# Performance work log

Measured on AMD Instinct MI355X. Metric: run time of the kernel, lower is better.

## Reference

```python
import jax, jax.numpy as jnp
import numpy as np

N = 100000   # nodes
E = 800000   # edges
D = 128      # input dim
H = 128      # hidden dim
C = 2        # output classes
BN_EPS = 1e-5


def setup_inputs() -> dict:
    key = jax.random.key(0)
    ks = jax.random.split(key, 24)
    glorot = lambda k, shape: jax.random.normal(k, shape, dtype=jnp.float32) * np.sqrt(2.0 / (shape[0] + shape[1]))
    inp = {
        "x": jax.random.normal(ks[0], (N, D), dtype=jnp.float32),
        "edge_index": jax.random.randint(ks[1], (2, E), 0, N, dtype=jnp.int64),
        "W0": glorot(ks[2], (D, H)), "b0": jnp.zeros((H,), jnp.float32),
        "W1": glorot(ks[3], (H, H)), "b1": jnp.zeros((H,), jnp.float32),
        "W2": glorot(ks[4], (H, H)), "b2": jnp.zeros((H,), jnp.float32),
        "W3": glorot(ks[5], (H, C)), "b3": jnp.zeros((C,), jnp.float32),
        # BatchNorm (eval mode: running stats)
        "bn0_g": jax.random.normal(ks[6], (H,), dtype=jnp.float32) * 0.1 + 1.0,
        "bn0_b": jax.random.normal(ks[7], (H,), dtype=jnp.float32) * 0.1,
        "bn0_m": jax.random.normal(ks[8], (H,), dtype=jnp.float32) * 0.1,
        "bn0_v": jax.random.uniform(ks[9], (H,), dtype=jnp.float32) + 0.5,
        "bn1_g": jax.random.normal(ks[10], (H,), dtype=jnp.float32) * 0.1 + 1.0,
        "bn1_b": jax.random.normal(ks[11], (H,), dtype=jnp.float32) * 0.1,
        "bn1_m": jax.random.normal(ks[12], (H,), dtype=jnp.float32) * 0.1,
        "bn1_v": jax.random.uniform(ks[13], (H,), dtype=jnp.float32) + 0.5,
    }
    return inp


def _gcn_conv(h, W, b, src, dst, norm, self_norm):
    # GCNConv: D^-1/2 (A + I) D^-1/2 (h W) + b
    hw = h @ W                                             # [N, out]
    msg = hw[src] * norm[:, None]                          # [E, out] gather
    agg = jax.ops.segment_sum(msg, dst, num_segments=N)    # [N, out] scatter-add
    return agg + hw * self_norm[:, None] + b


def _bn_eval(h, g, b, m, v):
    return (h - m) * (g * jax.lax.rsqrt(v + BN_EPS)) + b


def reference(x, edge_index, W0, b0, W1, b1, W2, b2, W3, b3,
              bn0_g, bn0_b, bn0_m, bn0_v, bn1_g, bn1_b, bn1_m, bn1_v):
    src, dst = edge_index[0], edge_index[1]
    # symmetric normalization with self-loops
    deg = jax.ops.segment_sum(jnp.ones((E,), jnp.float32), dst, num_segments=N) + 1.0
    dis = jax.lax.rsqrt(deg)                 # deg >= 1, no inf
    norm = dis[src] * dis[dst]               # per-edge norm
    self_norm = dis * dis                    # self-loop norm

    # layer 0 (eval mode: dropout is identity)
    h = jax.nn.relu(_gcn_conv(x, W0, b0, src, dst, norm, self_norm))
    # layer 1: conv -> bn -> relu -> residual
    h_prev = h
    h = _gcn_conv(h, W1, b1, src, dst, norm, self_norm)
    h = jax.nn.relu(_bn_eval(h, bn0_g, bn0_b, bn0_m, bn0_v)) + h_prev
    # layer 2
    h_prev = h
    h = _gcn_conv(h, W2, b2, src, dst, norm, self_norm)
    h = jax.nn.relu(_bn_eval(h, bn1_g, bn1_b, bn1_m, bn1_v)) + h_prev
    # output layer
    h = _gcn_conv(h, W3, b3, src, dst, norm, self_norm)
    return jax.nn.log_softmax(h, axis=1)
```

## Files before the change

kernel.cpp:

```cpp
#include <hip/hip_runtime.h>
#include <hip/hip_bf16.h>
#include <type_traits>

#define NN 100000
#define NE 800000
#define HD 128
#define BN_EPS 1e-5f
#define NB_E_C 3125

typedef __bf16 bf16x8 __attribute__((ext_vector_type(8)));
typedef __bf16 bf16x2 __attribute__((ext_vector_type(2)));
typedef float  f32x4  __attribute__((ext_vector_type(4)));
typedef float  f32x2  __attribute__((ext_vector_type(2)));


__global__ __launch_bounds__(256) void count_prep_k(const int* __restrict__ ei, int* __restrict__ count,
                                                    int* __restrict__ rank,
                                                    const float* __restrict__ W0, const float* __restrict__ W1,
                                                    const float* __restrict__ W2, __bf16* __restrict__ WT,
                                                    const float* __restrict__ g0, const float* __restrict__ b0,
                                                    const float* __restrict__ m0, const float* __restrict__ v0,
                                                    const float* __restrict__ g1, const float* __restrict__ b1,
                                                    const float* __restrict__ m1, const float* __restrict__ v1,
                                                    float* __restrict__ A0, float* __restrict__ B0,
                                                    float* __restrict__ A1, float* __restrict__ B1) {
    int bid = blockIdx.x;
    int tid = threadIdx.x;
    if (bid < NB_E_C) {
        int e = bid * 256 + tid;
        if (e < NE) rank[e] = atomicAdd(&count[ei[NE + e]], 1);
    } else if (bid < NB_E_C + 3) {
        int w = bid - NB_E_C;
        const float* Ws[3] = {W0, W1, W2};
        const float* W = Ws[w];
        __bf16* T = WT + w * (HD * HD);
        #pragma unroll 4
        for (int it = 0; it < 64; ++it) {
            int idx = it * 256 + tid;
            int n = idx >> 7, k = idx & 127;
            T[idx] = (__bf16)W[k * HD + n];
        }
    } else {
        if (tid < 128) {
            float a = g0[tid] * rsqrtf(v0[tid] + BN_EPS);
            A0[tid] = a; B0[tid] = b0[tid] - m0[tid] * a;
        } else {
            int u = tid - 128;
            float a = g1[u] * rsqrtf(v1[u] + BN_EPS);
            A1[u] = a; B1[u] = b1[u] - m1[u] * a;
        }
    }
}

__global__ __launch_bounds__(256) void scan1_k(const int* __restrict__ count,
                                               int* __restrict__ rp, int* __restrict__ bsums,
                                               float* __restrict__ dis, float* __restrict__ selfn) {
    __shared__ int sm[256];
    int tid = threadIdx.x;
    int i = blockIdx.x * 256 + tid;
    int v = (i < NN) ? count[i] : 0;
    if (i < NN) {
        float deg = (float)v + 1.0f;
        float di = rsqrtf(deg);
        dis[i] = di;
        selfn[i] = di * di;
    }
    sm[tid] = v; __syncthreads();
    for (int off = 1; off < 256; off <<= 1) {
        int t = (tid >= off) ? sm[tid - off] : 0;
        __syncthreads();
        sm[tid] += t;
        __syncthreads();
    }
    if (i < NN) rp[i] = sm[tid] - v;
    if (tid == 255) bsums[blockIdx.x] = sm[tid];
}

__global__ __launch_bounds__(256) void scan23_k(int* __restrict__ rp, const int* __restrict__ bsums, int nb) {
    __shared__ int sm[256];
    int tid = threadIdx.x;
    int b = blockIdx.x;
    int partial = 0;
    for (int i = tid; i < b; i += 256) partial += bsums[i];
    sm[tid] = partial; __syncthreads();
    #pragma unroll
    for (int off = 128; off > 0; off >>= 1) {
        if (tid < off) sm[tid] += sm[tid + off];
        __syncthreads();
    }
    int prefix = sm[0];
    int i = b * 256 + tid;
    if (i < NN) rp[i] += prefix;
    if (i == 0) rp[NN] = NE;
}

__global__ __launch_bounds__(256) void scatter_k(const int* __restrict__ ei, const int* __restrict__ rp,
                                                 const int* __restrict__ rank, const float* __restrict__ dis,
                                                 uint2* __restrict__ edges) {
    int e = blockIdx.x * 256 + threadIdx.x;
    if (e >= NE) return;
    int s = ei[e], d = ei[NE + e];
    int pos = rp[d] + rank[e];
    edges[pos] = make_uint2((unsigned)s, __float_as_uint(dis[s] * dis[d]));
}


template <typename T>
__global__ __launch_bounds__(256, 5) void gemm128_k(const T* __restrict__ A, const __bf16* __restrict__ WTg,
                                                    __bf16* __restrict__ HW) {
    __shared__ __bf16 WL[128 * 128];
    const int tid = threadIdx.x;
    const int wid  = __builtin_amdgcn_readfirstlane(tid >> 6);
    const int lane = tid & 63;
    const int m = lane & 15, quad = lane >> 4;
    const int row_base = blockIdx.x * 64 + wid * 16;

    int r = row_base + m;
    if (r >= NN) r = NN - 1;
    bf16x8 afr[4];
    if constexpr (std::is_same<T, float>::value) {
        const float4* ap = (const float4*)(A + (size_t)r * HD);
        #pragma unroll
        for (int ks = 0; ks < 4; ++ks) {
            float4 x0 = ap[ks * 8 + quad * 2], x1 = ap[ks * 8 + quad * 2 + 1];
            bf16x8 a;
            a[0] = (__bf16)x0.x; a[1] = (__bf16)x0.y; a[2] = (__bf16)x0.z; a[3] = (__bf16)x0.w;
            a[4] = (__bf16)x1.x; a[5] = (__bf16)x1.y; a[6] = (__bf16)x1.z; a[7] = (__bf16)x1.w;
            afr[ks] = a;
        }
    } else {
        const bf16x8* ap = (const bf16x8*)(A + (size_t)r * HD);
        #pragma unroll
        for (int ks = 0; ks < 4; ++ks) afr[ks] = ap[ks * 4 + quad];
    }

    #pragma unroll
    for (int it = 0; it < 8; ++it) {
        int id = it * 256 + tid;
        int n = id >> 4, c = id & 15;
        int cs = c ^ (n >> 3);
        *(uint4*)&WL[n * 128 + cs * 8] = *(const uint4*)(WTg + n * HD + c * 8);
    }
    __syncthreads();

    f32x4 acc[8];
    #pragma unroll
    for (int ct = 0; ct < 8; ++ct) acc[ct] = (f32x4){0.f, 0.f, 0.f, 0.f};

    #pragma unroll
    for (int ks = 0; ks < 4; ++ks) {
        #pragma unroll
        for (int ct = 0; ct < 8; ++ct) {
            int n = m * 8 + ct;
            int cs = (ks * 4 + quad) ^ m;
            bf16x8 bfr = *(const bf16x8*)&WL[n * 128 + cs * 8];
            acc[ct] = __builtin_amdgcn_mfma_f32_16x16x32_bf16(afr[ks], bfr, acc[ct], 0, 0, 0);
        }
    }

    #pragma unroll
    for (int rr = 0; rr < 4; ++rr) {
        int row = row_base + quad * 4 + rr;
        if (row < NN) {
            bf16x8 v;
            #pragma unroll
            for (int ct = 0; ct < 8; ++ct) v[ct] = (__bf16)acc[ct][rr];
            *(bf16x8*)(HW + (size_t)row * HD + m * 8) = v;
        }
    }
}


__device__ __forceinline__ void acc8p(f32x2* acc, uint4 rv, float wt) {
    f32x2 w2 = {wt, wt};
    f32x2 x0 = {__uint_as_float(rv.x << 16), __uint_as_float(rv.x & 0xffff0000u)};
    f32x2 x1 = {__uint_as_float(rv.y << 16), __uint_as_float(rv.y & 0xffff0000u)};
    f32x2 x2 = {__uint_as_float(rv.z << 16), __uint_as_float(rv.z & 0xffff0000u)};
    f32x2 x3 = {__uint_as_float(rv.w << 16), __uint_as_float(rv.w & 0xffff0000u)};
    acc[0] = __builtin_elementwise_fma(x0, w2, acc[0]);
    acc[1] = __builtin_elementwise_fma(x1, w2, acc[1]);
    acc[2] = __builtin_elementwise_fma(x2, w2, acc[2]);
    acc[3] = __builtin_elementwise_fma(x3, w2, acc[3]);
}


__global__ __launch_bounds__(256) void agg0_k(const __bf16* __restrict__ hw, const int* __restrict__ rp,
                                              const uint2* __restrict__ edges,
                                              const float* __restrict__ selfn, const float* __restrict__ bias,
                                              __bf16* __restrict__ hb) {
    const int lane = threadIdx.x & 63;
    const int wid  = threadIdx.x >> 6;
    const int grp  = lane >> 4;
    const int m    = lane & 15;
    const int n = blockIdx.x * 16 + wid * 4 + grp;
    const int c0 = m * 8;
    const int L = NE - 1;

    const int e0 = rp[n], e1 = rp[n + 1];
    const float sn = selfn[n];
    uint4 rv_self = *(const uint4*)(hw + ((size_t)n << 7) + c0);

    f32x2 acc2[4];
    #pragma unroll
    for (int j = 0; j < 4; ++j) acc2[j] = (f32x2){0.f, 0.f};

    int e = e0;
    int cnt = e1 - e0;
    uint2 edA = edges[min(e,     L)];
    uint2 edB = edges[min(e + 1, L)];
    uint2 edC = edges[min(e + 2, L)];
    uint2 edD = edges[min(e + 3, L)];
    while (cnt >= 4) {
        uint4 r0 = *(const uint4*)(hw + ((size_t)edA.x << 7) + c0);
        uint4 r1 = *(const uint4*)(hw + ((size_t)edB.x << 7) + c0);
        uint4 r2 = *(const uint4*)(hw + ((size_t)edC.x << 7) + c0);
        uint4 r3 = *(const uint4*)(hw + ((size_t)edD.x << 7) + c0);
        uint2 nA = edges[min(e + 4, L)];
        uint2 nB = edges[min(e + 5, L)];
        uint2 nC = edges[min(e + 6, L)];
        uint2 nD = edges[min(e + 7, L)];
        acc8p(acc2, r0, __uint_as_float(edA.y));
        acc8p(acc2, r1, __uint_as_float(edB.y));
        acc8p(acc2, r2, __uint_as_float(edC.y));
        acc8p(acc2, r3, __uint_as_float(edD.y));
        edA = nA; edB = nB; edC = nC; edD = nD;
        e += 4; cnt -= 4;
    }
    if (cnt >= 2) {
        uint4 r0 = *(const uint4*)(hw + ((size_t)edA.x << 7) + c0);
        uint4 r1 = *(const uint4*)(hw + ((size_t)edB.x << 7) + c0);
        acc8p(acc2, r0, __uint_as_float(edA.y));
        acc8p(acc2, r1, __uint_as_float(edB.y));
        edA = edC;
        cnt -= 2;
    }
    if (cnt == 1) {
        uint4 rv = *(const uint4*)(hw + ((size_t)edA.x << 7) + c0);
        acc8p(acc2, rv, __uint_as_float(edA.y));
    }
    acc8p(acc2, rv_self, sn);

    float a8[8] = {acc2[0][0], acc2[0][1], acc2[1][0], acc2[1][1],
                   acc2[2][0], acc2[2][1], acc2[3][0], acc2[3][1]};
    float4 bs0 = *(const float4*)(bias + c0);
    float4 bs1 = *(const float4*)(bias + c0 + 4);
    float bf[8] = {bs0.x, bs0.y, bs0.z, bs0.w, bs1.x, bs1.y, bs1.z, bs1.w};
    bf16x8 v;
    #pragma unroll
    for (int j = 0; j < 8; ++j) v[j] = (__bf16)fmaxf(a8[j] + bf[j], 0.f);
    *(bf16x8*)(hb + ((size_t)n << 7) + c0) = v;
}


template <int MODE>
__global__ __launch_bounds__(256, 5) void aggw_k(const __bf16* __restrict__ hbI, const __bf16* __restrict__ WTg,
                                                 const int* __restrict__ rp, const uint2* __restrict__ edges,
                                                 const float* __restrict__ selfn, const float* __restrict__ bias,
                                                 const float* __restrict__ bnA, const float* __restrict__ bnB,
                                                 __bf16* __restrict__ hbO, const float* __restrict__ W3,
                                                 float2* __restrict__ hw3) {
    __shared__ __bf16 SL[16 * 128];
    __shared__ __bf16 SelfL[16 * 128];
    const int tid = threadIdx.x;
    const int wid  = __builtin_amdgcn_readfirstlane(tid >> 6);
    const int lane = tid & 63;
    const int quad = lane >> 4;
    const int m    = lane & 15;
    const int nn = wid * 4 + quad;
    const int n = blockIdx.x * 16 + nn;
    const int c0 = m * 8;
    const int L = NE - 1;

    const int e0 = rp[n], e1 = rp[n + 1];
    const float sn = selfn[n];
    uint4 rv_self = *(const uint4*)(hbI + ((size_t)n << 7) + c0);

    bf16x8 wfr[2][4];
    #pragma unroll
    for (int t = 0; t < 2; ++t) {
        const __bf16* wp = WTg + (m * 8 + wid * 2 + t) * HD + quad * 8;
        #pragma unroll
        for (int ks = 0; ks < 4; ++ks)
            wfr[t][ks] = *(const bf16x8*)(wp + ks * 32);
    }

    f32x2 acc2[4];
    #pragma unroll
    for (int j = 0; j < 4; ++j) acc2[j] = (f32x2){0.f, 0.f};

    int e = e0;
    int cnt = e1 - e0;
    uint2 edA = edges[min(e,     L)];
    uint2 edB = edges[min(e + 1, L)];
    uint2 edC = edges[min(e + 2, L)];
    uint2 edD = edges[min(e + 3, L)];
    while (cnt >= 4) {
        uint4 r0 = *(const uint4*)(hbI + ((size_t)edA.x << 7) + c0);
        uint4 r1 = *(const uint4*)(hbI + ((size_t)edB.x << 7) + c0);
        uint4 r2 = *(const uint4*)(hbI + ((size_t)edC.x << 7) + c0);
        uint4 r3 = *(const uint4*)(hbI + ((size_t)edD.x << 7) + c0);
        uint2 nA = edges[min(e + 4, L)];
        uint2 nB = edges[min(e + 5, L)];
        uint2 nC = edges[min(e + 6, L)];
        uint2 nD = edges[min(e + 7, L)];
        acc8p(acc2, r0, __uint_as_float(edA.y));
        acc8p(acc2, r1, __uint_as_float(edB.y));
        acc8p(acc2, r2, __uint_as_float(edC.y));
        acc8p(acc2, r3, __uint_as_float(edD.y));
        edA = nA; edB = nB; edC = nC; edD = nD;
        e += 4; cnt -= 4;
    }
    if (cnt >= 2) {
        uint4 r0 = *(const uint4*)(hbI + ((size_t)edA.x << 7) + c0);
        uint4 r1 = *(const uint4*)(hbI + ((size_t)edB.x << 7) + c0);
        acc8p(acc2, r0, __uint_as_float(edA.y));
        acc8p(acc2, r1, __uint_as_float(edB.y));
        edA = edC;
        cnt -= 2;
    }
    if (cnt == 1) {
        uint4 rv = *(const uint4*)(hbI + ((size_t)edA.x << 7) + c0);
        acc8p(acc2, rv, __uint_as_float(edA.y));
    }
    acc8p(acc2, rv_self, sn);

    {
        float a8[8] = {acc2[0][0], acc2[0][1], acc2[1][0], acc2[1][1],
                       acc2[2][0], acc2[2][1], acc2[3][0], acc2[3][1]};
        bf16x8 sv;
        #pragma unroll
        for (int j = 0; j < 8; ++j) sv[j] = (__bf16)a8[j];
        int pc = m ^ nn;
        *(bf16x8*)&SL[nn * 128 + pc * 8] = sv;
        *(uint4*)&SelfL[nn * 128 + pc * 8] = rv_self;
    }
    __syncthreads();

    bf16x8 afr[4];
    #pragma unroll
    for (int ks = 0; ks < 4; ++ks) {
        int pcR = (ks * 4 + quad) ^ m;
        afr[ks] = *(const bf16x8*)&SL[m * 128 + pcR * 8];
    }
    f32x4 acc[2];
    acc[0] = (f32x4){0.f, 0.f, 0.f, 0.f};
    acc[1] = (f32x4){0.f, 0.f, 0.f, 0.f};
    #pragma unroll
    for (int ks = 0; ks < 4; ++ks) {
        #pragma unroll
        for (int t = 0; t < 2; ++t)
            acc[t] = __builtin_amdgcn_mfma_f32_16x16x32_bf16(afr[ks], wfr[t][ks], acc[t], 0, 0, 0);
    }

    const int ch0 = m * 8 + wid * 2;
    float2 bias2 = *(const float2*)(bias + ch0);
    float2 A2 = *(const float2*)(bnA + ch0);
    float2 B2 = *(const float2*)(bnB + ch0);
    float4 w3r;
    if (MODE == 2) w3r = *(const float4*)(W3 + ch0 * 2);
    float p0a[4], p1a[4];
    #pragma unroll
    for (int rr = 0; rr < 4; ++rr) {
        int nd = quad * 4 + rr;
        char* sp = (char*)SelfL + nd * 256 + ((m ^ nd) * 16) + wid * 4;
        unsigned sv = *(const unsigned*)sp;
        float s0 = __uint_as_float(sv << 16);
        float s1 = __uint_as_float(sv & 0xffff0000u);
        float z0 = acc[0][rr] + bias2.x;
        float z1 = acc[1][rr] + bias2.y;
        float h0 = fmaxf(fmaf(z0, A2.x, B2.x), 0.f) + s0;
        float h1 = fmaxf(fmaf(z1, A2.y, B2.y), 0.f) + s1;
        if (MODE == 1) {
            bf16x2 pr = {(__bf16)h0, (__bf16)h1};
            *(bf16x2*)sp = pr;
        } else {
            p0a[rr] = h0 * w3r.x + h1 * w3r.z;
            p1a[rr] = h0 * w3r.y + h1 * w3r.w;
        }
    }

    if (MODE == 1) {
        __syncthreads();
        uint4 outv = *(const uint4*)&SelfL[nn * 128 + (m ^ nn) * 8];
        *(uint4*)(hbO + ((size_t)n << 7) + c0) = outv;
    } else {
        #pragma unroll
        for (int rr = 0; rr < 4; ++rr) {
            #pragma unroll
            for (int o = 1; o < 16; o <<= 1) {
                p0a[rr] += __shfl_xor(p0a[rr], o);
                p1a[rr] += __shfl_xor(p1a[rr], o);
            }
        }
        __syncthreads();
        float2* PL = (float2*)SL;
        if (m == 0) {
            #pragma unroll
            for (int rr = 0; rr < 4; ++rr)
                PL[(quad * 4 + rr) * 4 + wid] = make_float2(p0a[rr], p1a[rr]);
        }
        __syncthreads();
        if (tid < 16) {
            float2 a = PL[tid * 4 + 0], b = PL[tid * 4 + 1];
            float2 c = PL[tid * 4 + 2], d = PL[tid * 4 + 3];
            hw3[blockIdx.x * 16 + tid] = make_float2(a.x + b.x + c.x + d.x,
                                                     a.y + b.y + c.y + d.y);
        }
    }
}


__global__ __launch_bounds__(256) void final_k(const float2* __restrict__ hw3, const int* __restrict__ rp,
                                               const uint2* __restrict__ edges,
                                               const float* __restrict__ selfn, const float* __restrict__ b3,
                                               float* __restrict__ out) {
    int n = blockIdx.x * 256 + threadIdx.x;
    if (n >= NN) return;
    const int L = NE - 1;
    float a0 = 0.f, a1 = 0.f;
    int e0 = rp[n], e1 = rp[n + 1];
    int cnt = e1 - e0;
    uint2 edA = edges[min(e0,     L)];
    uint2 edB = edges[min(e0 + 1, L)];
    int e = e0;
    while (cnt >= 2) {
        float2 v0 = hw3[edA.x];
        float2 v1 = hw3[edB.x];
        float w0 = __uint_as_float(edA.y), w1 = __uint_as_float(edB.y);
        edA = edges[min(e + 2, L)];
        edB = edges[min(e + 3, L)];
        a0 = fmaf(w0, v0.x, a0); a1 = fmaf(w0, v0.y, a1);
        a0 = fmaf(w1, v1.x, a0); a1 = fmaf(w1, v1.y, a1);
        e += 2; cnt -= 2;
    }
    if (cnt == 1) {
        float2 v = hw3[edA.x];
        float w = __uint_as_float(edA.y);
        a0 = fmaf(w, v.x, a0); a1 = fmaf(w, v.y, a1);
    }
    float sn = selfn[n];
    float2 hv = hw3[n];
    float z0 = a0 + sn * hv.x + b3[0];
    float z1 = a1 + sn * hv.y + b3[1];
    float mx = fmaxf(z0, z1);
    float l = mx + logf(expf(z0 - mx) + expf(z1 - mx));
    out[n * 2 + 0] = z0 - l;
    out[n * 2 + 1] = z1 - l;
}


extern "C" void kernel_launch(void* const* d_in, const int* in_sizes, int n_in,
                              void* d_out, int out_size, void* d_ws, size_t ws_size,
                              hipStream_t stream) {
    (void)in_sizes; (void)n_in; (void)out_size; (void)ws_size;

    const float* x   = (const float*)d_in[0];
    const int*   ei  = (const int*)d_in[1];
    const float* W0  = (const float*)d_in[2];
    const float* b0  = (const float*)d_in[3];
    const float* W1  = (const float*)d_in[4];
    const float* b1  = (const float*)d_in[5];
    const float* W2  = (const float*)d_in[6];
    const float* b2  = (const float*)d_in[7];
    const float* W3  = (const float*)d_in[8];
    const float* b3  = (const float*)d_in[9];
    const float* bn0g = (const float*)d_in[10];
    const float* bn0b = (const float*)d_in[11];
    const float* bn0m = (const float*)d_in[12];
    const float* bn0v = (const float*)d_in[13];
    const float* bn1g = (const float*)d_in[14];
    const float* bn1b = (const float*)d_in[15];
    const float* bn1m = (const float*)d_in[16];
    const float* bn1v = (const float*)d_in[17];
    float* out = (float*)d_out;

    char* p = (char*)d_ws;
    auto alloc = [&](size_t bytes) -> void* {
        void* r = (void*)p;
        p += (bytes + 255) & ~(size_t)255;
        return r;
    };
    __bf16*  hb    = (__bf16*)alloc((size_t)NN * HD * 2);
    __bf16*  hb2   = (__bf16*)alloc((size_t)NN * HD * 2);
    __bf16*  hw    = (__bf16*)alloc((size_t)NN * HD * 2);
    float2*  hw3   = (float2*)alloc((size_t)NN * 8);
    float*   dis   = (float*)alloc((size_t)NN * 4);
    float*   selfn = (float*)alloc((size_t)NN * 4);
    int*     count = (int*)alloc((size_t)NN * 4);
    int*     rp    = (int*)alloc((size_t)(NN + 1) * 4);
    uint2*   edges = (uint2*)alloc((size_t)NE * 8);
    int*     rank  = (int*)alloc((size_t)NE * 4);
    int*     bsums = (int*)alloc((size_t)512 * 4);
    float*   bnA0  = (float*)alloc(128 * 4);
    float*   bnB0  = (float*)alloc(128 * 4);
    float*   bnA1  = (float*)alloc(128 * 4);
    float*   bnB1  = (float*)alloc(128 * 4);
    __bf16*  WT    = (__bf16*)alloc((size_t)3 * HD * HD * 2);

    const int NB_N = (NN + 255) / 256;
    const int NB_G = (NN + 63) / 64;
    const int NB_A = (NN + 15) / 16;

    hipMemsetAsync(count, 0, (size_t)NN * 4, stream);

    count_prep_k<<<NB_E_C + 4, 256, 0, stream>>>(ei, count, rank,
                                                 W0, W1, W2, WT,
                                                 bn0g, bn0b, bn0m, bn0v, bn1g, bn1b, bn1m, bn1v,
                                                 bnA0, bnB0, bnA1, bnB1);
    scan1_k<<<NB_N, 256, 0, stream>>>(count, rp, bsums, dis, selfn);
    scan23_k<<<NB_N, 256, 0, stream>>>(rp, bsums, NB_N);
    scatter_k<<<NB_E_C, 256, 0, stream>>>(ei, rp, rank, dis, edges);

    gemm128_k<float><<<NB_G, 256, 0, stream>>>(x, WT, hw);
    agg0_k<<<NB_A, 256, 0, stream>>>(hw, rp, edges, selfn, b0, hb);
    aggw_k<1><<<NB_A, 256, 0, stream>>>(hb, WT + HD * HD, rp, edges, selfn, b1,
                                        bnA0, bnB0, hb2, nullptr, nullptr);
    aggw_k<2><<<NB_A, 256, 0, stream>>>(hb2, WT + 2 * HD * HD, rp, edges, selfn, b2,
                                        bnA1, bnB1, nullptr, W3, hw3);
    final_k<<<NB_N, 256, 0, stream>>>(hw3, rp, edges, selfn, b3, out);
}
```

Baseline: 333.0 us.

## Make aggregate-then-transform kernel wave-local, removing block barriers

Each wave now runs the dense transform on only its own 4 nodes, so the 16-row MFMA operand replicates those 4 rows. This lets the block-wide __syncthreads calls be replaced by wave-local lgkmcnt waits, and the final two-class projection is reduced inside the wave instead of across waves. The trade-off is that each wave loops over all 128 output channels, with 4x redundant MFMA work and weight fragments reloaded from global memory per channel tile. Launch bounds occupancy is also lowered from 5 to 4.

```diff
diff --git a/kernel.cpp b/kernel.cpp
--- a/kernel.cpp
+++ b/kernel.cpp
@@ -253,7 +253,7 @@
 
 
 template <int MODE>
-__global__ __launch_bounds__(256, 5) void aggw_k(const __bf16* __restrict__ hbI, const __bf16* __restrict__ WTg,
+__global__ __launch_bounds__(256, 4) void aggw_k(const __bf16* __restrict__ hbI, const __bf16* __restrict__ WTg,
                                                  const int* __restrict__ rp, const uint2* __restrict__ edges,
                                                  const float* __restrict__ selfn, const float* __restrict__ bias,
                                                  const float* __restrict__ bnA, const float* __restrict__ bnB,
@@ -262,27 +262,20 @@
     __shared__ __bf16 SL[16 * 128];
     __shared__ __bf16 SelfL[16 * 128];
     const int tid = threadIdx.x;
-    const int wid  = __builtin_amdgcn_readfirstlane(tid >> 6);
+    const int wid  = tid >> 6;
     const int lane = tid & 63;
-    const int quad = lane >> 4;
+    const int grp  = lane >> 4;
     const int m    = lane & 15;
-    const int nn = wid * 4 + quad;
-    const int n = blockIdx.x * 16 + nn;
+    const int nw   = wid * 4;
+    const int n = blockIdx.x * 16 + nw + grp;
     const int c0 = m * 8;
     const int L = NE - 1;
+    __bf16* SLw    = SL + nw * 128;
+    __bf16* SelfLw = SelfL + nw * 128;
 
     const int e0 = rp[n], e1 = rp[n + 1];
     const float sn = selfn[n];
     uint4 rv_self = *(const uint4*)(hbI + ((size_t)n << 7) + c0);
-
-    bf16x8 wfr[2][4];
-    #pragma unroll
-    for (int t = 0; t < 2; ++t) {
-        const __bf16* wp = WTg + (m * 8 + wid * 2 + t) * HD + quad * 8;
-        #pragma unroll
-        for (int ks = 0; ks < 4; ++ks)
-            wfr[t][ks] = *(const bf16x8*)(wp + ks * 32);
-    }
 
     f32x2 acc2[4];
     #pragma unroll
@@ -330,58 +323,74 @@
         bf16x8 sv;
         #pragma unroll
         for (int j = 0; j < 8; ++j) sv[j] = (__bf16)a8[j];
-        int pc = m ^ nn;
-        *(bf16x8*)&SL[nn * 128 + pc * 8] = sv;
-        *(uint4*)&SelfL[nn * 128 + pc * 8] = rv_self;
-    }
-    __syncthreads();
-
+        int pc = m ^ grp;
+        *(bf16x8*)&SLw[grp * 128 + pc * 8] = sv;
+        *(uint4*)&SelfLw[grp * 128 + pc * 8] = rv_self;
+    }
+    asm volatile("s_waitcnt lgkmcnt(0)" ::: "memory");
+    __builtin_amdgcn_sched_barrier(0);
+
+    const int an = m & 3;
     bf16x8 afr[4];
     #pragma unroll
     for (int ks = 0; ks < 4; ++ks) {
-        int pcR = (ks * 4 + quad) ^ m;
-        afr[ks] = *(const bf16x8*)&SL[m * 128 + pcR * 8];
-    }
-    f32x4 acc[2];
-    acc[0] = (f32x4){0.f, 0.f, 0.f, 0.f};
-    acc[1] = (f32x4){0.f, 0.f, 0.f, 0.f};
-    #pragma unroll
-    for (int ks = 0; ks < 4; ++ks) {
+        int pcR = (ks * 4 + grp) ^ an;
+        afr[ks] = *(const bf16x8*)&SLw[an * 128 + pcR * 8];
+    }
+
+    float4 bs0 = *(const float4*)(bias + c0);
+    float4 bs1 = *(const float4*)(bias + c0 + 4);
+    float4 a0v = *(const float4*)(bnA + c0), a1v = *(const float4*)(bnA + c0 + 4);
+    float4 b0v = *(const float4*)(bnB + c0), b1v = *(const float4*)(bnB + c0 + 4);
+    float bf[8] = {bs0.x, bs0.y, bs0.z, bs0.w, bs1.x, bs1.y, bs1.z, bs1.w};
+    float Af[8] = {a0v.x, a0v.y, a0v.z, a0v.w, a1v.x, a1v.y, a1v.z, a1v.w};
+    float Bf[8] = {b0v.x, b0v.y, b0v.z, b0v.w, b1v.x, b1v.y, b1v.z, b1v.w};
+    float w3f[16];
+    float p0a[4] = {0.f, 0.f, 0.f, 0.f}, p1a[4] = {0.f, 0.f, 0.f, 0.f};
+    if (MODE == 2) {
+        const float4* wp3 = (const float4*)(W3 + m * 16);
         #pragma unroll
-        for (int t = 0; t < 2; ++t)
-            acc[t] = __builtin_amdgcn_mfma_f32_16x16x32_bf16(afr[ks], wfr[t][ks], acc[t], 0, 0, 0);
-    }
-
-    const int ch0 = m * 8 + wid * 2;
-    float2 bias2 = *(const float2*)(bias + ch0);
-    float2 A2 = *(const float2*)(bnA + ch0);
-    float2 B2 = *(const float2*)(bnB + ch0);
-    float4 w3r;
-    if (MODE == 2) w3r = *(const float4*)(W3 + ch0 * 2);
-    float p0a[4], p1a[4];
-    #pragma unroll
-    for (int rr = 0; rr < 4; ++rr) {
-        int nd = quad * 4 + rr;
-        char* sp = (char*)SelfL + nd * 256 + ((m ^ nd) * 16) + wid * 4;
-        unsigned sv = *(const unsigned*)sp;
-        float s0 = __uint_as_float(sv << 16);
-        float s1 = __uint_as_float(sv & 0xffff0000u);
-        float z0 = acc[0][rr] + bias2.x;
-        float z1 = acc[1][rr] + bias2.y;
-        float h0 = fmaxf(fmaf(z0, A2.x, B2.x), 0.f) + s0;
-        float h1 = fmaxf(fmaf(z1, A2.y, B2.y), 0.f) + s1;
-        if (MODE == 1) {
-            bf16x2 pr = {(__bf16)h0, (__bf16)h1};
-            *(bf16x2*)sp = pr;
-        } else {
-            p0a[rr] = h0 * w3r.x + h1 * w3r.z;
-            p1a[rr] = h0 * w3r.y + h1 * w3r.w;
+        for (int j = 0; j < 4; ++j) {
+            float4 t = wp3[j];
+            w3f[j * 4] = t.x; w3f[j * 4 + 1] = t.y; w3f[j * 4 + 2] = t.z; w3f[j * 4 + 3] = t.w;
+        }
+    }
+
+    #pragma unroll 2
+    for (int ct = 0; ct < 8; ++ct) {
+        const __bf16* wp = WTg + (c0 + ct) * HD + grp * 8;
+        bf16x8 w0f = *(const bf16x8*)(wp);
+        bf16x8 w1f = *(const bf16x8*)(wp + 32);
+        bf16x8 w2f = *(const bf16x8*)(wp + 64);
+        bf16x8 w3fr = *(const bf16x8*)(wp + 96);
+        f32x4 acc = (f32x4){0.f, 0.f, 0.f, 0.f};
+        acc = __builtin_amdgcn_mfma_f32_16x16x32_bf16(afr[0], w0f, acc, 0, 0, 0);
+        acc = __builtin_amdgcn_mfma_f32_16x16x32_bf16(afr[1], w1f, acc, 0, 0, 0);
+        acc = __builtin_amdgcn_mfma_f32_16x16x32_bf16(afr[2], w2f, acc, 0, 0, 0);
+        acc = __builtin_amdgcn_mfma_f32_16x16x32_bf16(afr[3], w3fr, acc, 0, 0, 0);
+
+        if (grp == 0) {
+            #pragma unroll
+            for (int rr = 0; rr < 4; ++rr) {
+                char* sp = (char*)SelfLw + rr * 256 + ((m ^ rr) * 16) + ct * 2;
+                unsigned short us = *(const unsigned short*)sp;
+                float s0 = __uint_as_float(((unsigned)us) << 16);
+                float z = acc[rr] + bf[ct];
+                float h = fmaxf(fmaf(z, Af[ct], Bf[ct]), 0.f) + s0;
+                if (MODE == 1) {
+                    *(__bf16*)sp = (__bf16)h;
+                } else {
+                    p0a[rr] = fmaf(h, w3f[2 * ct], p0a[rr]);
+                    p1a[rr] = fmaf(h, w3f[2 * ct + 1], p1a[rr]);
+                }
+            }
         }
     }
 
     if (MODE == 1) {
-        __syncthreads();
-        uint4 outv = *(const uint4*)&SelfL[nn * 128 + (m ^ nn) * 8];
+        asm volatile("s_waitcnt lgkmcnt(0)" ::: "memory");
+        __builtin_amdgcn_sched_barrier(0);
+        uint4 outv = *(const uint4*)&SelfLw[grp * 128 + ((m ^ grp) * 8)];
         *(uint4*)(hbO + ((size_t)n << 7) + c0) = outv;
     } else {
         #pragma unroll
@@ -392,19 +401,10 @@
                 p1a[rr] += __shfl_xor(p1a[rr], o);
             }
         }
-        __syncthreads();
-        float2* PL = (float2*)SL;
-        if (m == 0) {
-            #pragma unroll
-            for (int rr = 0; rr < 4; ++rr)
-                PL[(quad * 4 + rr) * 4 + wid] = make_float2(p0a[rr], p1a[rr]);
-        }
-        __syncthreads();
-        if (tid < 16) {
-            float2 a = PL[tid * 4 + 0], b = PL[tid * 4 + 1];
-            float2 c = PL[tid * 4 + 2], d = PL[tid * 4 + 3];
-            hw3[blockIdx.x * 16 + tid] = make_float2(a.x + b.x + c.x + d.x,
-                                                     a.y + b.y + c.y + d.y);
+        if (lane < 4) {
+            float q0 = (lane == 0) ? p0a[0] : (lane == 1) ? p0a[1] : (lane == 2) ? p0a[2] : p0a[3];
+            float q1 = (lane == 0) ? p1a[0] : (lane == 1) ? p1a[1] : (lane == 2) ? p1a[2] : p1a[3];
+            hw3[blockIdx.x * 16 + nw + lane] = make_float2(q0, q1);
         }
     }
 }
```

Result: slower. 468.2 us (+40.6%).
